# Kernel tuning notes

Measured on AMD Instinct MI355X. Metric: run time of the kernel, lower is better.

The kernel has to match this reference:

```python
import jax, jax.numpy as jnp
import numpy as np

C_IN, C_HID, H, C_Z = 256, 32, 8, 128
N_SEQ, N_RES = 128, 384
INF = 1e9


def layer_norm(x, w, b, eps=1e-5):
    mu = jnp.mean(x, axis=-1, keepdims=True)
    var = jnp.var(x, axis=-1, keepdims=True)
    return (x - mu) * jax.lax.rsqrt(var + eps) * w + b


def setup_inputs() -> dict:
    key = jax.random.key(0)
    ks = jax.random.split(key, 12)
    s = 0.02
    return {
        "m": jax.random.normal(ks[0], (N_SEQ, N_RES, C_IN), jnp.float32),
        "z": jax.random.normal(ks[1], (N_RES, N_RES, C_Z), jnp.float32),
        "mask": jnp.ones((N_SEQ, N_RES), jnp.float32),
        "ln_m_w": jnp.ones((C_IN,), jnp.float32),
        "ln_m_b": jnp.zeros((C_IN,), jnp.float32),
        "ln_z_w": jnp.ones((C_Z,), jnp.float32),
        "ln_z_b": jnp.zeros((C_Z,), jnp.float32),
        "w_pair": jax.random.normal(ks[2], (C_Z, H), jnp.float32) * s,
        "wq": jax.random.normal(ks[3], (C_IN, H, C_HID), jnp.float32) * s,
        "wk": jax.random.normal(ks[4], (C_IN, H, C_HID), jnp.float32) * s,
        "wv": jax.random.normal(ks[5], (C_IN, H, C_HID), jnp.float32) * s,
        "wg": jax.random.normal(ks[6], (C_IN, H, C_HID), jnp.float32) * s,
        "bg": jnp.ones((H, C_HID), jnp.float32),
        "wo": jax.random.normal(ks[7], (H * C_HID, C_IN), jnp.float32) * s,
        "bo": jnp.zeros((C_IN,), jnp.float32),
    }


def reference(m, z, mask, ln_m_w, ln_m_b, ln_z_w, ln_z_b, w_pair,
              wq, wk, wv, wg, bg, wo, bo):
    # [N_seq, N_res, C_in]
    m_ln = layer_norm(m, ln_m_w, ln_m_b)

    # mask bias: [N_seq, 1, 1, N_res]
    bias = (INF * (mask - 1.0))[:, None, None, :]
    # pair bias: layernorm(z) -> [N_res, N_res, H] -> [1, H, N_res, N_res]
    z_ln = layer_norm(z, ln_z_w, ln_z_b)
    pair_b = jnp.einsum("qkc,ch->hqk", z_ln, w_pair)[None]
    bias = bias + pair_b  # [N_seq, H, N_res, N_res]

    scale = C_HID ** -0.5
    q = jnp.einsum("sqc,chd->sqhd", m_ln, wq) * scale
    k = jnp.einsum("skc,chd->skhd", m_ln, wk)
    v = jnp.einsum("skc,chd->skhd", m_ln, wv)

    logits = jnp.einsum("sqhd,skhd->shqk", q, k) + bias
    a = jax.nn.softmax(logits, axis=-1)
    o = jnp.einsum("shqk,skhd->sqhd", a, v)

    g = jax.nn.sigmoid(jnp.einsum("sqc,chd->sqhd", m_ln, wg) + bg)
    o = (o * g).reshape(N_SEQ, N_RES, H * C_HID)
    return jnp.einsum("sqe,ec->sqc", o, wo) + bo
```

## Files before the change

### kernel.cpp

```cpp
#include <hip/hip_runtime.h>
#include <hip/hip_bf16.h>

#define S 128
#define R 384
#define CIN 256
#define H 8
#define D 32
#define CZ 128
#define E 256

typedef __attribute__((ext_vector_type(8))) short short8;
typedef __attribute__((ext_vector_type(4))) short short4_;
typedef __attribute__((ext_vector_type(4))) float f32x4;
typedef __attribute__((ext_vector_type(4))) unsigned int u32x4;

union U8 { short8 s; unsigned int u[4]; };

__device__ __forceinline__ unsigned short f2bs_u(float f) {
    __hip_bfloat16 h = __float2bfloat16(f);
    return *reinterpret_cast<unsigned short*>(&h);
}
__device__ __forceinline__ short f2bs(float f) {
    __hip_bfloat16 h = __float2bfloat16(f);
    return *reinterpret_cast<short*>(&h);
}
__device__ __forceinline__ float bs2f(unsigned short u) {
    union { unsigned int i; float f; } c;
    c.i = ((unsigned int)u) << 16;
    return c.f;
}
__device__ __forceinline__ unsigned int packhl(float x) {
    unsigned short h = f2bs_u(x);
    float rem = x - bs2f(h);
    unsigned short l = f2bs_u(rem);
    return (unsigned int)h | ((unsigned int)l << 16);
}
__device__ __forceinline__ void xpose4(float& x0, float& x1, float& x2, float& x3, int p) {
    float tmp;
    if (p & 1) { tmp = x0; x0 = x1; x1 = tmp; tmp = x2; x2 = x3; x3 = tmp; }
    x1 = __shfl_xor(x1, 1); x3 = __shfl_xor(x3, 1);
    if (p & 1) { tmp = x0; x0 = x1; x1 = tmp; tmp = x2; x2 = x3; x3 = tmp; }
    if (p & 2) { tmp = x0; x0 = x2; x2 = tmp; tmp = x1; x1 = x3; x3 = tmp; }
    x2 = __shfl_xor(x2, 2); x3 = __shfl_xor(x3, 2);
    if (p & 2) { tmp = x0; x0 = x2; x2 = tmp; tmp = x1; x1 = x3; x3 = tmp; }
}

__global__ __launch_bounds__(256) void k_prepw(
    const float* __restrict__ wq, const float* __restrict__ wk,
    const float* __restrict__ wv, const float* __restrict__ wg,
    const float* __restrict__ wo,
    unsigned short* __restrict__ wt_hi, unsigned short* __restrict__ wt_lo,
    unsigned short* __restrict__ wot_hi, unsigned short* __restrict__ wot_lo)
{
    __shared__ float tl[32][36];
    const int b = blockIdx.x, t = threadIdx.x;
    const int iswo = (b >= 256);
    const int bb = iswo ? (b - 256) : (b & 63);
    const int te = bb >> 3, tc = bb & 7;
    const int mat = b >> 6;
    const float* src = iswo ? wo : (mat == 0 ? wq : mat == 1 ? wk : mat == 2 ? wv : wg);
    unsigned short* dh = iswo ? wot_hi : wt_hi + (size_t)mat * 65536;
    unsigned short* dl = iswo ? wot_lo : wt_lo + (size_t)mat * 65536;

    const int r = t >> 3, c4 = (t & 7) * 4;
    float4 v = *(const float4*)(src + (size_t)(tc * 32 + r) * 256 + te * 32 + c4);
    tl[r][c4] = v.x; tl[r][c4 + 1] = v.y; tl[r][c4 + 2] = v.z; tl[r][c4 + 3] = v.w;
    __syncthreads();
    short4_ hv, lv;
#pragma unroll
    for (int j = 0; j < 4; j++) {
        float x = tl[c4 + j][r];
        unsigned short hb = f2bs_u(x);
        hv[j] = (short)hb;
        lv[j] = f2bs(x - bs2f(hb));
    }
    size_t o = (size_t)(te * 32 + r) * 256 + tc * 32 + c4;
    *(short4_*)(dh + o) = hv;
    *(short4_*)(dl + o) = lv;
}

__global__ __launch_bounds__(256) void k_pairbias(
    const float* __restrict__ z, const float* __restrict__ lnw,
    const float* __restrict__ lnb, const float* __restrict__ wp,
    float* __restrict__ pb)
{
    int wid  = blockIdx.x * 4 + (threadIdx.x >> 6);
    int lane = threadIdx.x & 63;
    int qi = wid / R;
    int ki = wid - qi * R;
    const float* zr = z + (size_t)wid * CZ;
    float z0 = zr[lane], z1 = zr[lane + 64];
    float s  = z0 + z1;
    float sq = z0 * z0 + z1 * z1;
#pragma unroll
    for (int off = 32; off >= 1; off >>= 1) {
        s  += __shfl_xor(s, off);
        sq += __shfl_xor(sq, off);
    }
    float mu   = s * (1.0f / CZ);
    float var  = sq * (1.0f / CZ) - mu * mu;
    float rstd = rsqrtf(var + 1e-5f);
    float zl0 = (z0 - mu) * rstd * lnw[lane]      + lnb[lane];
    float zl1 = (z1 - mu) * rstd * lnw[lane + 64] + lnb[lane + 64];
    const float* w0 = wp + lane * H;
    const float* w1 = wp + (lane + 64) * H;
    float ph[H];
#pragma unroll
    for (int h = 0; h < H; h++) ph[h] = zl0 * w0[h] + zl1 * w1[h];
#pragma unroll
    for (int off = 32; off >= 1; off >>= 1) {
#pragma unroll
        for (int h = 0; h < H; h++) ph[h] += __shfl_xor(ph[h], off);
    }
    if (lane == 0) {
#pragma unroll
        for (int h = 0; h < H; h++)
            pb[((size_t)h * R + qi) * R + ki] = ph[h];
    }
}

__global__ __launch_bounds__(256, 2) void k_proj(
    const float* __restrict__ m, const float* __restrict__ lnw,
    const float* __restrict__ lnb,
    const unsigned short* __restrict__ wt_hi, const unsigned short* __restrict__ wt_lo,
    const float* __restrict__ bg,
    unsigned short* __restrict__ qb, unsigned short* __restrict__ kb,
    unsigned short* __restrict__ vtb, float* __restrict__ gb)
{
    __shared__ unsigned int mtb[64][260];
    __shared__ float red[2][4][64];
    __shared__ float muv[64][2];
    const int t = threadIdx.x;
    const int row0 = blockIdx.x * 64;
    const int sblk = blockIdx.x / 6;
    const int res0 = (blockIdx.x % 6) * 64;

#pragma unroll
    for (int i = 0; i < 16; i++) {
        int e4 = i * 256 + t;
        int r = e4 >> 6, c = (e4 & 63) * 4;
        f32x4 v = *(const f32x4*)(m + (size_t)(row0 + r) * CIN + c);
        *(f32x4*)&mtb[r][c] = v;
    }
    __syncthreads();
    {
        int row = t & 63, j = t >> 6;
        float s = 0.f, sq = 0.f;
#pragma unroll
        for (int i = 0; i < 16; i++) {
            f32x4 v = *(const f32x4*)&mtb[row][j * 64 + i * 4];
#pragma unroll
            for (int q = 0; q < 4; q++) { s += v[q]; sq += v[q] * v[q]; }
        }
        red[0][j][row] = s; red[1][j][row] = sq;
    }
    __syncthreads();
    if (t < 64) {
        float s  = red[0][0][t] + red[0][1][t] + red[0][2][t] + red[0][3][t];
        float sq = red[1][0][t] + red[1][1][t] + red[1][2][t] + red[1][3][t];
        float mu  = s * (1.0f / CIN);
        float var = sq * (1.0f / CIN) - mu * mu;
        muv[t][0] = mu;
        muv[t][1] = rsqrtf(var + 1e-5f);
    }
    __syncthreads();
    {
        float lw = lnw[t], lb = lnb[t];
#pragma unroll 8
        for (int r = 0; r < 64; r++) {
            union { unsigned int i; float f; } c;
            c.i = mtb[r][t];
            float y = (c.f - muv[r][0]) * muv[r][1] * lw + lb;
            mtb[r][t] = packhl(y);
        }
    }
    __syncthreads();

    const int w = t >> 6, lane = t & 63, ln = lane & 15, quad = lane >> 4;
    const unsigned short* Bh = wt_hi + (size_t)w * 65536;
    const unsigned short* Bl = wt_lo + (size_t)w * 65536;

    for (int nc = 0; nc < 4; nc++) {
        const int nbase = nc * 64;
        f32x4 acc[4][4];
#pragma unroll
        for (int a = 0; a < 4; a++)
#pragma unroll
            for (int b = 0; b < 4; b++) acc[a][b] = (f32x4){0.f, 0.f, 0.f, 0.f};

        for (int kk = 0; kk < 8; kk++) {
            const int kcol = kk * 32 + quad * 8;
            short8 ah[4], al[4];
#pragma unroll
            for (int mt = 0; mt < 4; mt++) {
                const unsigned int* up = &mtb[mt * 16 + ln][kcol];
                u32x4 u0 = *(const u32x4*)up;
                u32x4 u1 = *(const u32x4*)(up + 4);
                U8 A, L;
                A.u[0] = (u0[0] & 0xffffu) | (u0[1] << 16);
                A.u[1] = (u0[2] & 0xffffu) | (u0[3] << 16);
                A.u[2] = (u1[0] & 0xffffu) | (u1[1] << 16);
                A.u[3] = (u1[2] & 0xffffu) | (u1[3] << 16);
                L.u[0] = (u0[0] >> 16) | (u0[1] & 0xffff0000u);
                L.u[1] = (u0[2] >> 16) | (u0[3] & 0xffff0000u);
                L.u[2] = (u1[0] >> 16) | (u1[1] & 0xffff0000u);
                L.u[3] = (u1[2] >> 16) | (u1[3] & 0xffff0000u);
                ah[mt] = A.s; al[mt] = L.s;
            }
#pragma unroll
            for (int nt = 0; nt < 4; nt++) {
                size_t boff = (size_t)(nbase + nt * 16 + ln) * 256 + kcol;
                short8 bh = *(const short8*)(Bh + boff);
                short8 bl = *(const short8*)(Bl + boff);
#pragma unroll
                for (int mt = 0; mt < 4; mt++) {
                    acc[mt][nt] = __builtin_amdgcn_mfma_f32_16x16x32_bf16(ah[mt], bh, acc[mt][nt], 0, 0, 0);
                    acc[mt][nt] = __builtin_amdgcn_mfma_f32_16x16x32_bf16(al[mt], bh, acc[mt][nt], 0, 0, 0);
                    acc[mt][nt] = __builtin_amdgcn_mfma_f32_16x16x32_bf16(ah[mt], bl, acc[mt][nt], 0, 0, 0);
                }
            }
        }
        if (w == 2) {
#pragma unroll
            for (int mt = 0; mt < 4; mt++) {
                int resg = res0 + mt * 16 + quad * 4;
#pragma unroll
                for (int nt = 0; nt < 4; nt++) {
                    int e = nbase + nt * 16 + ln;
                    int hh = e >> 5, d = e & 31;
                    f32x4 a = acc[mt][nt];
                    short4_ vv;
                    vv[0] = f2bs(a[0]); vv[1] = f2bs(a[1]);
                    vv[2] = f2bs(a[2]); vv[3] = f2bs(a[3]);
                    *(short4_*)(vtb + (((size_t)(sblk * H + hh)) * D + d) * R + resg) = vv;
                }
            }
        } else if (w == 3) {
            const int p = ln & 3;
#pragma unroll
            for (int mt = 0; mt < 4; mt++) {
                int rowg = row0 + mt * 16 + quad * 4 + p;
#pragma unroll
                for (int nt = 0; nt < 4; nt++) {
                    int e0 = nbase + nt * 16 + (ln & 12);
                    f32x4 a = acc[mt][nt];
                    float x0 = a[0], x1 = a[1], x2 = a[2], x3 = a[3];
                    xpose4(x0, x1, x2, x3, p);
                    float4 bgv = *(const float4*)(bg + e0);
                    f32x4 g;
                    g[0] = 1.0f / (1.0f + __expf(-(x0 + bgv.x)));
                    g[1] = 1.0f / (1.0f + __expf(-(x1 + bgv.y)));
                    g[2] = 1.0f / (1.0f + __expf(-(x2 + bgv.z)));
                    g[3] = 1.0f / (1.0f + __expf(-(x3 + bgv.w)));
                    *(f32x4*)(gb + (size_t)rowg * E + e0) = g;
                }
            }
        } else {
            const float sc = (w == 0) ? 0.17677669529663687f : 1.0f;
            unsigned short* dst = (w == 0) ? qb : kb;
            const int p = ln & 3;
#pragma unroll
            for (int mt = 0; mt < 4; mt++) {
                int resg = res0 + mt * 16 + quad * 4 + p;
#pragma unroll
                for (int nt = 0; nt < 4; nt++) {
                    int e0 = nbase + nt * 16 + (ln & 12);
                    f32x4 a = acc[mt][nt];
                    float x0 = a[0] * sc, x1 = a[1] * sc, x2 = a[2] * sc, x3 = a[3] * sc;
                    xpose4(x0, x1, x2, x3, p);
                    int hh = e0 >> 5, d0 = e0 & 31;
                    short4_ vv;
                    vv[0] = f2bs(x0); vv[1] = f2bs(x1); vv[2] = f2bs(x2); vv[3] = f2bs(x3);
                    *(short4_*)(dst + (((size_t)(sblk * H + hh)) * R + resg) * D + d0) = vv;
                }
            }
        }
    }
}

__global__ __launch_bounds__(256, 2) void k_attn(
    const unsigned short* __restrict__ qb, const unsigned short* __restrict__ kb,
    const unsigned short* __restrict__ vtb, const float* __restrict__ gb,
    const float* __restrict__ pb, const float* __restrict__ mask,
    float* __restrict__ og)
{
    __shared__ unsigned short Ks[R][40];
    __shared__ unsigned short Vt[D][392];
    __shared__ float Ps[4][16][100];
    const int t = threadIdx.x;
    const int s = blockIdx.x >> 3;
    const int h = blockIdx.x & 7;
    const size_t kvbase = (size_t)(s * H + h) * R * D;

#pragma unroll
    for (int i = 0; i < 6; i++) {
        int idx = i * 256 + t;
        int res = idx >> 2, d = (idx & 3) * 8;
        *(short8*)&Ks[res][d] = *(const short8*)(kb + kvbase + (size_t)res * D + d);
    }
#pragma unroll
    for (int i = 0; i < 6; i++) {
        int idx = i * 256 + t;
        int d = idx / 48, j = idx - d * 48;
        *(short8*)&Vt[d][j * 8] = *(const short8*)(vtb + kvbase + (size_t)d * R + j * 8);
    }
    __syncthreads();

    const int w = t >> 6;
    const int lane = t & 63;
    const int ln = lane & 15;
    const int quad = lane >> 4;
    float (*Pw)[100] = Ps[w];

    float mr[24];
#pragma unroll
    for (int tt = 0; tt < 24; tt++)
        mr[tt] = 1e9f * (mask[s * R + tt * 16 + ln] - 1.0f);

    for (int qt = 0; qt < 6; qt++) {
        const int q0 = w * 96 + qt * 16;
        short8 aq = *(const short8*)(qb + kvbase + (size_t)(q0 + ln) * D + quad * 8);
        const float* pbrow = pb + ((size_t)h * R + q0 + quad * 4) * R + ln;

        f32x4 acc[24];
#pragma unroll
        for (int tt = 0; tt < 24; tt++) {
            f32x4 c;
#pragma unroll
            for (int r = 0; r < 4; r++)
                c[r] = pbrow[(size_t)r * R + tt * 16] + mr[tt];
            short8 bk = *(const short8*)&Ks[tt * 16 + ln][quad * 8];
            acc[tt] = __builtin_amdgcn_mfma_f32_16x16x32_bf16(aq, bk, c, 0, 0, 0);
        }
        float l[4];
#pragma unroll
        for (int r = 0; r < 4; r++) {
            float mx = acc[0][r];
#pragma unroll
            for (int tt = 1; tt < 24; tt++) mx = fmaxf(mx, acc[tt][r]);
            mx = fmaxf(mx, __shfl_xor(mx, 1));
            mx = fmaxf(mx, __shfl_xor(mx, 2));
            mx = fmaxf(mx, __shfl_xor(mx, 4));
            mx = fmaxf(mx, __shfl_xor(mx, 8));
            float sum = 0.f;
#pragma unroll
            for (int tt = 0; tt < 24; tt++) {
                float p = __expf(acc[tt][r] - mx);
                acc[tt][r] = p;
                sum += p;
            }
            sum += __shfl_xor(sum, 1);
            sum += __shfl_xor(sum, 2);
            sum += __shfl_xor(sum, 4);
            sum += __shfl_xor(sum, 8);
            l[r] = sum;
        }
        f32x4 o0 = {0.f, 0.f, 0.f, 0.f}, o1 = {0.f, 0.f, 0.f, 0.f};
        for (int cc = 0; cc < 4; cc++) {
#pragma unroll
            for (int tt6 = 0; tt6 < 6; tt6++) {
                int tt = cc * 6 + tt6;
#pragma unroll
                for (int r = 0; r < 4; r++)
                    Pw[quad * 4 + r][tt6 * 16 + ln] = acc[tt][r];
            }
#pragma unroll
            for (int kk = 0; kk < 3; kk++) {
                f32x4 plo = *(f32x4*)&Pw[ln][kk * 32 + quad * 8];
                f32x4 phi = *(f32x4*)&Pw[ln][kk * 32 + quad * 8 + 4];
                short8 ap;
#pragma unroll
                for (int j = 0; j < 4; j++) {
                    ap[j]     = f2bs(plo[j]);
                    ap[4 + j] = f2bs(phi[j]);
                }
                int kg = cc * 96 + kk * 32;
                short8 bv0 = *(const short8*)&Vt[ln][kg + quad * 8];
                short8 bv1 = *(const short8*)&Vt[16 + ln][kg + quad * 8];
                o0 = __builtin_amdgcn_mfma_f32_16x16x32_bf16(ap, bv0, o0, 0, 0, 0);
                o1 = __builtin_amdgcn_mfma_f32_16x16x32_bf16(ap, bv1, o1, 0, 0, 0);
            }
        }
#pragma unroll
        for (int r = 0; r < 4; r++) {
            int mrow = quad * 4 + r;
            int rw = s * R + q0 + mrow;
            float invl = 1.0f / l[r];
            size_t base = (size_t)rw * E + h * D;
            float g0 = gb[base + ln];
            float g1 = gb[base + 16 + ln];
            og[base + ln]      = o0[r] * invl * g0;
            og[base + 16 + ln] = o1[r] * invl * g1;
        }
    }
}

__global__ __launch_bounds__(256, 2) void k_outproj(
    const float* __restrict__ og, const unsigned short* __restrict__ wot_hi,
    const unsigned short* __restrict__ wot_lo, const float* __restrict__ bo,
    float* __restrict__ out)
{
    __shared__ unsigned int otb[64][260];
    const int t = threadIdx.x;
    const int row0 = blockIdx.x * 64;
#pragma unroll
    for (int i = 0; i < 16; i++) {
        int e4 = i * 256 + t;
        int r = e4 >> 6, c = (e4 & 63) * 4;
        f32x4 v = *(const f32x4*)(og + (size_t)(row0 + r) * E + c);
        u32x4 pk;
        pk[0] = packhl(v[0]); pk[1] = packhl(v[1]);
        pk[2] = packhl(v[2]); pk[3] = packhl(v[3]);
        *(u32x4*)&otb[r][c] = pk;
    }
    __syncthreads();

    const int w = t >> 6, lane = t & 63, ln = lane & 15, quad = lane >> 4;
    const int nbase = w * 64;
    f32x4 acc[4][4];
#pragma unroll
    for (int a = 0; a < 4; a++)
#pragma unroll
        for (int b = 0; b < 4; b++) acc[a][b] = (f32x4){0.f, 0.f, 0.f, 0.f};

    for (int kk = 0; kk < 8; kk++) {
        const int kcol = kk * 32 + quad * 8;
        short8 ah[4], al[4];
#pragma unroll
        for (int mt = 0; mt < 4; mt++) {
            const unsigned int* up = &otb[mt * 16 + ln][kcol];
            u32x4 u0 = *(const u32x4*)up;
            u32x4 u1 = *(const u32x4*)(up + 4);
            U8 A, L;
            A.u[0] = (u0[0] & 0xffffu) | (u0[1] << 16);
            A.u[1] = (u0[2] & 0xffffu) | (u0[3] << 16);
            A.u[2] = (u1[0] & 0xffffu) | (u1[1] << 16);
            A.u[3] = (u1[2] & 0xffffu) | (u1[3] << 16);
            L.u[0] = (u0[0] >> 16) | (u0[1] & 0xffff0000u);
            L.u[1] = (u0[2] >> 16) | (u0[3] & 0xffff0000u);
            L.u[2] = (u1[0] >> 16) | (u1[1] & 0xffff0000u);
            L.u[3] = (u1[2] >> 16) | (u1[3] & 0xffff0000u);
            ah[mt] = A.s; al[mt] = L.s;
        }
#pragma unroll
        for (int nt = 0; nt < 4; nt++) {
            size_t boff = (size_t)(nbase + nt * 16 + ln) * 256 + kcol;
            short8 bh = *(const short8*)(wot_hi + boff);
            short8 bl = *(const short8*)(wot_lo + boff);
#pragma unroll
            for (int mt = 0; mt < 4; mt++) {
                acc[mt][nt] = __builtin_amdgcn_mfma_f32_16x16x32_bf16(ah[mt], bh, acc[mt][nt], 0, 0, 0);
                acc[mt][nt] = __builtin_amdgcn_mfma_f32_16x16x32_bf16(al[mt], bh, acc[mt][nt], 0, 0, 0);
                acc[mt][nt] = __builtin_amdgcn_mfma_f32_16x16x32_bf16(ah[mt], bl, acc[mt][nt], 0, 0, 0);
            }
        }
    }
    const int p = ln & 3;
#pragma unroll
    for (int mt = 0; mt < 4; mt++) {
        int rowg = row0 + mt * 16 + quad * 4 + p;
#pragma unroll
        for (int nt = 0; nt < 4; nt++) {
            int c0 = nbase + nt * 16 + (ln & 12);
            f32x4 a = acc[mt][nt];
            float x0 = a[0], x1 = a[1], x2 = a[2], x3 = a[3];
            xpose4(x0, x1, x2, x3, p);
            float4 bov = *(const float4*)(bo + c0);
            f32x4 o;
            o[0] = x0 + bov.x; o[1] = x1 + bov.y;
            o[2] = x2 + bov.z; o[3] = x3 + bov.w;
            *(f32x4*)(out + (size_t)rowg * CIN + c0) = o;
        }
    }
}

extern "C" void kernel_launch(void* const* d_in, const int* in_sizes, int n_in,
                              void* d_out, int out_size, void* d_ws, size_t ws_size,
                              hipStream_t stream)
{
    const float* m      = (const float*)d_in[0];
    const float* z      = (const float*)d_in[1];
    const float* mask   = (const float*)d_in[2];
    const float* ln_m_w = (const float*)d_in[3];
    const float* ln_m_b = (const float*)d_in[4];
    const float* ln_z_w = (const float*)d_in[5];
    const float* ln_z_b = (const float*)d_in[6];
    const float* w_pair = (const float*)d_in[7];
    const float* wq     = (const float*)d_in[8];
    const float* wk     = (const float*)d_in[9];
    const float* wv     = (const float*)d_in[10];
    const float* wg     = (const float*)d_in[11];
    const float* bg     = (const float*)d_in[12];
    const float* wo     = (const float*)d_in[13];
    const float* bo     = (const float*)d_in[14];
    float* out = (float*)d_out;

    char* ws = (char*)d_ws;
    float*          pbuf   = (float*)ws;              ws += 4718592;
    unsigned short* qb     = (unsigned short*)ws;     ws += 25165824;
    unsigned short* kb     = (unsigned short*)ws;     ws += 25165824;
    unsigned short* vtb    = (unsigned short*)ws;     ws += 25165824;
    float*          gbuf   = (float*)ws;              ws += 50331648;
    float*          ogb    = (float*)ws;              ws += 50331648;
    unsigned short* wt_hi  = (unsigned short*)ws;     ws += 524288;
    unsigned short* wt_lo  = (unsigned short*)ws;     ws += 524288;
    unsigned short* wot_hi = (unsigned short*)ws;     ws += 131072;
    unsigned short* wot_lo = (unsigned short*)ws;     ws += 131072;

    k_prepw<<<dim3(320), dim3(256), 0, stream>>>(wq, wk, wv, wg, wo,
                                                 wt_hi, wt_lo, wot_hi, wot_lo);
    k_pairbias<<<dim3(R * R / 4), dim3(256), 0, stream>>>(z, ln_z_w, ln_z_b, w_pair, pbuf);
    k_proj<<<dim3(768), dim3(256), 0, stream>>>(m, ln_m_w, ln_m_b,
                                                wt_hi, wt_lo, bg, qb, kb, vtb, gbuf);
    k_attn<<<dim3(S * H), dim3(256), 0, stream>>>(qb, kb, vtb, gbuf, pbuf, mask, ogb);
    k_outproj<<<dim3(768), dim3(256), 0, stream>>>(ogb, wot_hi, wot_lo, bo, out);
}
```

Before: 525.5 us.

## Drop lo-split of LayerNorm activations in projection and store gate as bf16

The projection kernel now keeps the layer-normed activations as a single bf16 copy in shared memory instead of a packed hi/lo pair. This removes one of the three MFMAs per tile and the unpacking work. Row statistics are computed straight from global memory with a shuffle reduction, the smaller LDS footprint allows a higher occupancy hint, and the gate buffer is written and read as bf16, halving its traffic. The cost is lower precision in the activation operand and in the gate values.

New measurement: 496.6 us. 1.06x faster.

```diff
diff --git a/kernel.cpp b/kernel.cpp
--- a/kernel.cpp
+++ b/kernel.cpp
@@ -119,60 +119,55 @@
     }
 }
 
-__global__ __launch_bounds__(256, 2) void k_proj(
+__global__ __launch_bounds__(256, 3) void k_proj(
     const float* __restrict__ m, const float* __restrict__ lnw,
     const float* __restrict__ lnb,
     const unsigned short* __restrict__ wt_hi, const unsigned short* __restrict__ wt_lo,
     const float* __restrict__ bg,
     unsigned short* __restrict__ qb, unsigned short* __restrict__ kb,
-    unsigned short* __restrict__ vtb, float* __restrict__ gb)
-{
-    __shared__ unsigned int mtb[64][260];
-    __shared__ float red[2][4][64];
+    unsigned short* __restrict__ vtb, unsigned short* __restrict__ gb)
+{
+    __shared__ unsigned short Ah[64][264];
     __shared__ float muv[64][2];
     const int t = threadIdx.x;
     const int row0 = blockIdx.x * 64;
     const int sblk = blockIdx.x / 6;
     const int res0 = (blockIdx.x % 6) * 64;
 
+    if (t < 128) {
+        int r = t >> 1, half = t & 1;
+        const float* mr = m + (size_t)(row0 + r) * CIN + half * 128;
+        float s = 0.f, sq = 0.f;
+#pragma unroll
+        for (int i = 0; i < 32; i++) {
+            f32x4 v = *(const f32x4*)(mr + i * 4);
+#pragma unroll
+            for (int q = 0; q < 4; q++) { s += v[q]; sq += v[q] * v[q]; }
+        }
+        s  += __shfl_xor(s, 1);
+        sq += __shfl_xor(sq, 1);
+        if (half == 0) {
+            float mu  = s * (1.0f / CIN);
+            float var = sq * (1.0f / CIN) - mu * mu;
+            muv[r][0] = mu;
+            muv[r][1] = rsqrtf(var + 1e-5f);
+        }
+    }
+    __syncthreads();
 #pragma unroll
     for (int i = 0; i < 16; i++) {
-        int e4 = i * 256 + t;
-        int r = e4 >> 6, c = (e4 & 63) * 4;
-        f32x4 v = *(const f32x4*)(m + (size_t)(row0 + r) * CIN + c);
-        *(f32x4*)&mtb[r][c] = v;
-    }
-    __syncthreads();
-    {
-        int row = t & 63, j = t >> 6;
-        float s = 0.f, sq = 0.f;
-#pragma unroll
-        for (int i = 0; i < 16; i++) {
-            f32x4 v = *(const f32x4*)&mtb[row][j * 64 + i * 4];
-#pragma unroll
-            for (int q = 0; q < 4; q++) { s += v[q]; sq += v[q] * v[q]; }
-        }
-        red[0][j][row] = s; red[1][j][row] = sq;
-    }
-    __syncthreads();
-    if (t < 64) {
-        float s  = red[0][0][t] + red[0][1][t] + red[0][2][t] + red[0][3][t];
-        float sq = red[1][0][t] + red[1][1][t] + red[1][2][t] + red[1][3][t];
-        float mu  = s * (1.0f / CIN);
-        float var = sq * (1.0f / CIN) - mu * mu;
-        muv[t][0] = mu;
-        muv[t][1] = rsqrtf(var + 1e-5f);
-    }
-    __syncthreads();
-    {
-        float lw = lnw[t], lb = lnb[t];
-#pragma unroll 8
-        for (int r = 0; r < 64; r++) {
-            union { unsigned int i; float f; } c;
-            c.i = mtb[r][t];
-            float y = (c.f - muv[r][0]) * muv[r][1] * lw + lb;
-            mtb[r][t] = packhl(y);
-        }
+        int idx = i * 256 + t;
+        int r = idx >> 6, c4 = (idx & 63) * 4;
+        f32x4 v = *(const f32x4*)(m + (size_t)(row0 + r) * CIN + c4);
+        float4 lw = *(const float4*)(lnw + c4);
+        float4 lb = *(const float4*)(lnb + c4);
+        float mu = muv[r][0], rs = muv[r][1];
+        short4_ o;
+        o[0] = f2bs((v[0] - mu) * rs * lw.x + lb.x);
+        o[1] = f2bs((v[1] - mu) * rs * lw.y + lb.y);
+        o[2] = f2bs((v[2] - mu) * rs * lw.z + lb.z);
+        o[3] = f2bs((v[3] - mu) * rs * lw.w + lb.w);
+        *(short4_*)&Ah[r][c4] = o;
     }
     __syncthreads();
 
@@ -188,25 +183,13 @@
 #pragma unroll
             for (int b = 0; b < 4; b++) acc[a][b] = (f32x4){0.f, 0.f, 0.f, 0.f};
 
+#pragma unroll 2
         for (int kk = 0; kk < 8; kk++) {
             const int kcol = kk * 32 + quad * 8;
-            short8 ah[4], al[4];
-#pragma unroll
-            for (int mt = 0; mt < 4; mt++) {
-                const unsigned int* up = &mtb[mt * 16 + ln][kcol];
-                u32x4 u0 = *(const u32x4*)up;
-                u32x4 u1 = *(const u32x4*)(up + 4);
-                U8 A, L;
-                A.u[0] = (u0[0] & 0xffffu) | (u0[1] << 16);
-                A.u[1] = (u0[2] & 0xffffu) | (u0[3] << 16);
-                A.u[2] = (u1[0] & 0xffffu) | (u1[1] << 16);
-                A.u[3] = (u1[2] & 0xffffu) | (u1[3] << 16);
-                L.u[0] = (u0[0] >> 16) | (u0[1] & 0xffff0000u);
-                L.u[1] = (u0[2] >> 16) | (u0[3] & 0xffff0000u);
-                L.u[2] = (u1[0] >> 16) | (u1[1] & 0xffff0000u);
-                L.u[3] = (u1[2] >> 16) | (u1[3] & 0xffff0000u);
-                ah[mt] = A.s; al[mt] = L.s;
-            }
+            short8 ah[4];
+#pragma unroll
+            for (int mt = 0; mt < 4; mt++)
+                ah[mt] = *(const short8*)&Ah[mt * 16 + ln][kcol];
 #pragma unroll
             for (int nt = 0; nt < 4; nt++) {
                 size_t boff = (size_t)(nbase + nt * 16 + ln) * 256 + kcol;
@@ -215,7 +198,6 @@
 #pragma unroll
                 for (int mt = 0; mt < 4; mt++) {
                     acc[mt][nt] = __builtin_amdgcn_mfma_f32_16x16x32_bf16(ah[mt], bh, acc[mt][nt], 0, 0, 0);
-                    acc[mt][nt] = __builtin_amdgcn_mfma_f32_16x16x32_bf16(al[mt], bh, acc[mt][nt], 0, 0, 0);
                     acc[mt][nt] = __builtin_amdgcn_mfma_f32_16x16x32_bf16(ah[mt], bl, acc[mt][nt], 0, 0, 0);
                 }
             }
@@ -247,12 +229,12 @@
                     float x0 = a[0], x1 = a[1], x2 = a[2], x3 = a[3];
                     xpose4(x0, x1, x2, x3, p);
                     float4 bgv = *(const float4*)(bg + e0);
-                    f32x4 g;
-                    g[0] = 1.0f / (1.0f + __expf(-(x0 + bgv.x)));
-                    g[1] = 1.0f / (1.0f + __expf(-(x1 + bgv.y)));
-                    g[2] = 1.0f / (1.0f + __expf(-(x2 + bgv.z)));
-                    g[3] = 1.0f / (1.0f + __expf(-(x3 + bgv.w)));
-                    *(f32x4*)(gb + (size_t)rowg * E + e0) = g;
+                    short4_ gv;
+                    gv[0] = f2bs(1.0f / (1.0f + __expf(-(x0 + bgv.x))));
+                    gv[1] = f2bs(1.0f / (1.0f + __expf(-(x1 + bgv.y))));
+                    gv[2] = f2bs(1.0f / (1.0f + __expf(-(x2 + bgv.z))));
+                    gv[3] = f2bs(1.0f / (1.0f + __expf(-(x3 + bgv.w))));
+                    *(short4_*)(gb + (size_t)rowg * E + e0) = gv;
                 }
             }
         } else {
@@ -280,7 +262,7 @@
 
 __global__ __launch_bounds__(256, 2) void k_attn(
     const unsigned short* __restrict__ qb, const unsigned short* __restrict__ kb,
-    const unsigned short* __restrict__ vtb, const float* __restrict__ gb,
+    const unsigned short* __restrict__ vtb, const unsigned short* __restrict__ gb,
     const float* __restrict__ pb, const float* __restrict__ mask,
     float* __restrict__ og)
 {
@@ -387,8 +369,8 @@
             int rw = s * R + q0 + mrow;
             float invl = 1.0f / l[r];
             size_t base = (size_t)rw * E + h * D;
-            float g0 = gb[base + ln];
-            float g1 = gb[base + 16 + ln];
+            float g0 = bs2f(gb[base + ln]);
+            float g1 = bs2f(gb[base + 16 + ln]);
             og[base + ln]      = o0[r] * invl * g0;
             og[base + 16 + ln] = o1[r] * invl * g1;
         }
@@ -500,7 +482,7 @@
     unsigned short* qb     = (unsigned short*)ws;     ws += 25165824;
     unsigned short* kb     = (unsigned short*)ws;     ws += 25165824;
     unsigned short* vtb    = (unsigned short*)ws;     ws += 25165824;
-    float*          gbuf   = (float*)ws;              ws += 50331648;
+    unsigned short* gbuf   = (unsigned short*)ws;     ws += 25165824;
     float*          ogb    = (float*)ws;              ws += 50331648;
     unsigned short* wt_hi  = (unsigned short*)ws;     ws += 524288;
     unsigned short* wt_lo  = (unsigned short*)ws;     ws += 524288;
```
